# Kernel tuning notes

Measured on AMD Instinct MI355X. Metric: run time of the kernel, lower is better.

Reference implementation:

```python
import jax, jax.numpy as jnp
import numpy as np

BETA = 0.25  # commitment_beta from CodebookDecoder default


def setup_inputs() -> dict:
    key = jax.random.key(0)
    k1, k2, k3 = jax.random.split(key, 3)
    Q, B, K, D = 2048, 40000, 2048, 512
    return {
        "query_emb": jax.random.normal(k1, (Q, D), dtype=jnp.float32),
        "entity_emb": jax.random.normal(k2, (B, D), dtype=jnp.float32),
        "codebook": jax.random.normal(k3, (K, D), dtype=jnp.float32),
    }


def _quantize(x, codebook):
    # Nearest-neighbor lookup. torch.norm(x[:,None]-cb[None]) argmin is
    # equivalent to argmin of squared distance, expanded to avoid the
    x2 = jnp.sum(x * x, axis=1, keepdims=True)            # (B, 1)
    c2 = jnp.sum(codebook * codebook, axis=1)             # (K,)
    d2 = x2 - 2.0 * (x @ codebook.T) + c2[None, :]        # (B, K)
    idx = jnp.argmin(d2, axis=1)                          # (B,)
    quant = codebook[idx]                                 # (B, D) gather
    # vq_loss = mse(quant.detach(), x) + beta * mse(quant, x.detach())
    vq_loss = jnp.mean((jax.lax.stop_gradient(quant) - x) ** 2) \
        + BETA * jnp.mean((quant - jax.lax.stop_gradient(x)) ** 2)
    return quant, idx, vq_loss


def reference(query_emb, entity_emb, codebook):
    quant, idx, vq_loss = _quantize(entity_emb, codebook)
    score = query_emb @ quant.T                           # (Q, B)
    return score, vq_loss, idx
```

## Files before the change

kernel.cpp:

```cpp
#include <hip/hip_runtime.h>
#include <stdint.h>

#define Q    2048
#define NB   40000
#define NK   2048
#define ND   512
#define SCORE_SIZE (Q * NB)

typedef __bf16 bf16;
typedef bf16  bf16x8 __attribute__((ext_vector_type(8)));
typedef float f32x4  __attribute__((ext_vector_type(4)));

__device__ __forceinline__ unsigned short f2bf_rne(float f) {
    unsigned int u = __float_as_uint(f);
    u += 0x7FFFu + ((u >> 16) & 1u);
    return (unsigned short)(u >> 16);
}

__global__ __launch_bounds__(256) void c2_kernel(const float* __restrict__ cb,
                                                 float* __restrict__ c2) {
    int wave = threadIdx.x >> 6, lane = threadIdx.x & 63;
    int row  = blockIdx.x * 4 + wave;
    const float4* p = (const float4*)(cb + (size_t)row * ND);
    float4 a = p[lane];
    float4 b = p[lane + 64];
    float s = a.x*a.x + a.y*a.y + a.z*a.z + a.w*a.w
            + b.x*b.x + b.y*b.y + b.z*b.z + b.w*b.w;
    #pragma unroll
    for (int off = 32; off; off >>= 1) s += __shfl_down(s, off);
    if (lane == 0) c2[row] = s;
}

#define DPAD 132
__global__ __launch_bounds__(256) void dist_argmin_kernel(
        const float* __restrict__ ent, const float* __restrict__ cb,
        const float* __restrict__ c2g, float2* __restrict__ partial) {
    __shared__ float Es[32 * DPAD];
    __shared__ float Cs[32 * DPAD];
    int tid = threadIdx.x;
    int b0 = blockIdx.x * 128;
    int k0 = blockIdx.y * 128;
    int tx = tid & 15;
    int ty = tid >> 4;

    float acc[8][8] = {};

    for (int dc = 0; dc < ND; dc += 32) {
        __syncthreads();
        #pragma unroll
        for (int q = 0; q < 4; ++q) {
            int f4 = q * 256 + tid;
            int r  = f4 >> 3;
            int cc = f4 & 7;
            int br = b0 + r; br = br < NB ? br : NB - 1;
            float4 evv = *(const float4*)(ent + (size_t)br * ND + dc + cc * 4);
            float4 cvv = *(const float4*)(cb  + (size_t)(k0 + r) * ND + dc + cc * 4);
            int col = cc * 4;
            Es[(col + 0) * DPAD + r] = evv.x;
            Es[(col + 1) * DPAD + r] = evv.y;
            Es[(col + 2) * DPAD + r] = evv.z;
            Es[(col + 3) * DPAD + r] = evv.w;
            Cs[(col + 0) * DPAD + r] = cvv.x;
            Cs[(col + 1) * DPAD + r] = cvv.y;
            Cs[(col + 2) * DPAD + r] = cvv.z;
            Cs[(col + 3) * DPAD + r] = cvv.w;
        }
        __syncthreads();
        #pragma unroll 8
        for (int dd = 0; dd < 32; ++dd) {
            float4 e0 = *(const float4*)&Es[dd * DPAD + ty * 8];
            float4 e1 = *(const float4*)&Es[dd * DPAD + ty * 8 + 4];
            float4 q0 = *(const float4*)&Cs[dd * DPAD + tx * 8];
            float4 q1 = *(const float4*)&Cs[dd * DPAD + tx * 8 + 4];
            float ev[8] = {e0.x, e0.y, e0.z, e0.w, e1.x, e1.y, e1.z, e1.w};
            float cv[8] = {q0.x, q0.y, q0.z, q0.w, q1.x, q1.y, q1.z, q1.w};
            #pragma unroll
            for (int i = 0; i < 8; ++i)
                #pragma unroll
                for (int j = 0; j < 8; ++j)
                    acc[i][j] = fmaf(ev[i], cv[j], acc[i][j]);
        }
    }

    float c2v[8];
    #pragma unroll
    for (int j = 0; j < 8; ++j) c2v[j] = c2g[k0 + tx * 8 + j];

    for (int i = 0; i < 8; ++i) {
        int b = b0 + ty * 8 + i;
        float best = c2v[0] - 2.0f * acc[i][0];
        int bidx = k0 + tx * 8;
        #pragma unroll
        for (int j = 1; j < 8; ++j) {
            float v = c2v[j] - 2.0f * acc[i][j];
            if (v < best) { best = v; bidx = k0 + tx * 8 + j; }
        }
        #pragma unroll
        for (int off = 1; off < 16; off <<= 1) {
            float ov = __shfl_xor(best, off);
            int   oi = __shfl_xor(bidx, off);
            if (ov < best || (ov == best && oi < bidx)) { best = ov; bidx = oi; }
        }
        if (tx == 0 && b < NB)
            partial[(size_t)blockIdx.y * NB + b] = make_float2(best, __int_as_float(bidx));
    }
}

__global__ __launch_bounds__(256) void argmin_reduce_kernel(
        const float2* __restrict__ partial, int* __restrict__ idx_ws,
        float* __restrict__ out_idx) {
    int b = blockIdx.x * 256 + threadIdx.x;
    if (b >= NB) return;
    float2 p0 = partial[b];
    float best = p0.x;
    int bidx = __float_as_int(p0.y);
    #pragma unroll
    for (int t = 1; t < 16; ++t) {
        float2 p = partial[(size_t)t * NB + b];
        int i = __float_as_int(p.y);
        if (p.x < best || (p.x == best && i < bidx)) { best = p.x; bidx = i; }
    }
    idx_ws[b] = bidx;
    out_idx[b] = (float)bidx;
}

__global__ __launch_bounds__(256) void gather_loss_kernel(
        const float* __restrict__ ent, const float* __restrict__ cb,
        const int* __restrict__ idx_ws, unsigned short* __restrict__ quantb,
        float* __restrict__ acc) {
    int b = blockIdx.x;
    int k = idx_ws[b];
    int d = threadIdx.x * 2;
    float2 cv = *(const float2*)(cb  + (size_t)k * ND + d);
    float2 xv = *(const float2*)(ent + (size_t)b * ND + d);
    unsigned int packed = (unsigned int)f2bf_rne(cv.x) | ((unsigned int)f2bf_rne(cv.y) << 16);
    *(unsigned int*)(quantb + (size_t)b * ND + d) = packed;
    float dx = cv.x - xv.x, dy = cv.y - xv.y;
    float s = dx * dx + dy * dy;
    #pragma unroll
    for (int off = 32; off; off >>= 1) s += __shfl_down(s, off);
    __shared__ float wsum[4];
    int lane = threadIdx.x & 63, wave = threadIdx.x >> 6;
    if (lane == 0) wsum[wave] = s;
    __syncthreads();
    if (threadIdx.x == 0) atomicAdd(acc, wsum[0] + wsum[1] + wsum[2] + wsum[3]);
}

__global__ void vq_final_kernel(const float* __restrict__ acc, float* __restrict__ out) {
    out[0] = 1.25f * acc[0] / (float)(NB * ND);
}

__global__ __launch_bounds__(256) void qcvt_kernel(const float* __restrict__ qry,
                                                   unsigned short* __restrict__ qb) {
    int i = (blockIdx.x * 256 + threadIdx.x) * 4;
    float4 v = *(const float4*)(qry + i);
    uint2 u;
    u.x = (unsigned int)f2bf_rne(v.x) | ((unsigned int)f2bf_rne(v.y) << 16);
    u.y = (unsigned int)f2bf_rne(v.z) | ((unsigned int)f2bf_rne(v.w) << 16);
    *(uint2*)(qb + i) = u;
}

__global__ __launch_bounds__(256) void score_kernel(
        const unsigned short* __restrict__ Aq, const unsigned short* __restrict__ Bq,
        float* __restrict__ C) {
    __shared__ unsigned short As[128 * 32];
    __shared__ unsigned short Bs[128 * 32];
    int tid = threadIdx.x;
    int n0 = blockIdx.x * 128;
    int m0 = blockIdx.y * 128;
    int lane = tid & 63, wave = tid >> 6;
    int wm = wave >> 1, wn = wave & 1;
    int lr = lane & 15, quad = lane >> 4;

    f32x4 acc[4][4] = {};

    for (int kt = 0; kt < ND; kt += 32) {
        __syncthreads();
        #pragma unroll
        for (int r = 0; r < 2; ++r) {
            int e = r * 256 + tid;
            int row = e >> 2, cc = e & 3;
            uint4 va = *(const uint4*)(Aq + (size_t)(m0 + row) * ND + kt + cc * 8);
            *(uint4*)(As + row * 32 + cc * 8) = va;
            int nr = n0 + row; nr = nr < NB ? nr : NB - 1;
            uint4 vb = *(const uint4*)(Bq + (size_t)nr * ND + kt + cc * 8);
            *(uint4*)(Bs + row * 32 + cc * 8) = vb;
        }
        __syncthreads();
        bf16x8 af[4], bfr[4];
        #pragma unroll
        for (int mi = 0; mi < 4; ++mi)
            af[mi] = *(const bf16x8*)(As + (wm * 64 + mi * 16 + lr) * 32 + quad * 8);
        #pragma unroll
        for (int ni = 0; ni < 4; ++ni)
            bfr[ni] = *(const bf16x8*)(Bs + (wn * 64 + ni * 16 + lr) * 32 + quad * 8);
        #pragma unroll
        for (int mi = 0; mi < 4; ++mi)
            #pragma unroll
            for (int ni = 0; ni < 4; ++ni)
                acc[mi][ni] = __builtin_amdgcn_mfma_f32_16x16x32_bf16(
                    af[mi], bfr[ni], acc[mi][ni], 0, 0, 0);
    }

    #pragma unroll
    for (int mi = 0; mi < 4; ++mi) {
        #pragma unroll
        for (int ni = 0; ni < 4; ++ni) {
            int col = n0 + wn * 64 + ni * 16 + lr;
            if (col < NB) {
                #pragma unroll
                for (int r = 0; r < 4; ++r) {
                    int row = m0 + wm * 64 + mi * 16 + quad * 4 + r;
                    C[(size_t)row * NB + col] = acc[mi][ni][r];
                }
            }
        }
    }
}

extern "C" void kernel_launch(void* const* d_in, const int* in_sizes, int n_in,
                              void* d_out, int out_size, void* d_ws, size_t ws_size,
                              hipStream_t stream) {
    const float* qry = (const float*)d_in[0];
    const float* ent = (const float*)d_in[1];
    const float* cb  = (const float*)d_in[2];
    float* out = (float*)d_out;

    char* ws = (char*)d_ws;
    unsigned short* quantb = (unsigned short*)(ws);
    unsigned short* qb     = (unsigned short*)(ws + 40960000);
    float2*         partial= (float2*)(ws + 43057152);
    int*            idx_ws = (int*)(ws + 48177152);
    float*          c2     = (float*)(ws + 48337152);
    float*          acc    = (float*)(ws + 48345344);

    hipMemsetAsync(acc, 0, sizeof(float), stream);

    c2_kernel<<<NK / 4, 256, 0, stream>>>(cb, c2);
    dist_argmin_kernel<<<dim3(313, 16), 256, 0, stream>>>(ent, cb, c2, partial);
    argmin_reduce_kernel<<<(NB + 255) / 256, 256, 0, stream>>>(
        partial, idx_ws, out + SCORE_SIZE + 1);
    gather_loss_kernel<<<NB, 256, 0, stream>>>(ent, cb, idx_ws, quantb, acc);
    vq_final_kernel<<<1, 1, 0, stream>>>(acc, out + SCORE_SIZE);
    qcvt_kernel<<<1024, 256, 0, stream>>>(qry, qb);
    score_kernel<<<dim3(313, 16), 256, 0, stream>>>(qb, quantb, out);
}
```

Measured before the change: 1.990 ms.

## Compute codebook distances with split-bf16 MFMA, top-2 candidates, and exact fp32 rescoring

Replaces the scalar fp32 FMA distance GEMM with bf16 MFMA using a hi/lo split (three MFMAs per tile) to approximate fp32 accuracy. Each wave-half keeps its top-2 candidates, a merge kernel picks the top-4 per entity, and a rescore kernel recomputes exact fp32 distances to choose the final index, write the bf16 quant row and accumulate the loss. Entity pre-splitting into a workspace is used only when the workspace is large enough; otherwise the split happens on the fly during tile loads. This trades extra conversion passes and extra MFMA work for much higher matrix throughput, with a small risk of argmin mismatches if the true winner falls outside the candidate set.

Result: slower. 2.100 ms (+5.5%).

```diff
diff --git a/kernel.cpp b/kernel.cpp
--- a/kernel.cpp
+++ b/kernel.cpp
@@ -15,6 +15,17 @@
     unsigned int u = __float_as_uint(f);
     u += 0x7FFFu + ((u >> 16) & 1u);
     return (unsigned short)(u >> 16);
+}
+__device__ __forceinline__ float bf2f(unsigned short h) {
+    return __uint_as_float((unsigned int)h << 16);
+}
+__device__ __forceinline__ void split_pair_trunc(float x0, float x1,
+                                                 unsigned int& hp, unsigned int& lp) {
+    unsigned int u0 = __float_as_uint(x0), u1 = __float_as_uint(x1);
+    hp = (u0 >> 16) | (u1 & 0xFFFF0000u);
+    float l0 = x0 - __uint_as_float(u0 & 0xFFFF0000u);
+    float l1 = x1 - __uint_as_float(u1 & 0xFFFF0000u);
+    lp = (__float_as_uint(l0) >> 16) | (__float_as_uint(l1) & 0xFFFF0000u);
 }
 
 __global__ __launch_bounds__(256) void c2_kernel(const float* __restrict__ cb,
@@ -31,119 +42,222 @@
     if (lane == 0) c2[row] = s;
 }
 
-#define DPAD 132
-__global__ __launch_bounds__(256) void dist_argmin_kernel(
-        const float* __restrict__ ent, const float* __restrict__ cb,
-        const float* __restrict__ c2g, float2* __restrict__ partial) {
-    __shared__ float Es[32 * DPAD];
-    __shared__ float Cs[32 * DPAD];
+__global__ __launch_bounds__(256) void cvt_cb_kernel(const float* __restrict__ cb,
+        unsigned short* __restrict__ chi, unsigned short* __restrict__ clo) {
+    int i = (blockIdx.x * 256 + threadIdx.x) * 4;
+    float4 v = *(const float4*)(cb + i);
+    unsigned short h[4]; float l[4];
+    float x[4] = {v.x, v.y, v.z, v.w};
+    #pragma unroll
+    for (int j = 0; j < 4; ++j) { h[j] = f2bf_rne(x[j]); l[j] = x[j] - bf2f(h[j]); }
+    uint2 hp, lp;
+    hp.x = (unsigned int)h[0] | ((unsigned int)h[1] << 16);
+    hp.y = (unsigned int)h[2] | ((unsigned int)h[3] << 16);
+    lp.x = (unsigned int)f2bf_rne(l[0]) | ((unsigned int)f2bf_rne(l[1]) << 16);
+    lp.y = (unsigned int)f2bf_rne(l[2]) | ((unsigned int)f2bf_rne(l[3]) << 16);
+    *(uint2*)(chi + i) = hp;
+    *(uint2*)(clo + i) = lp;
+}
+
+__global__ __launch_bounds__(256) void cvt_ent_kernel(const float* __restrict__ ent,
+        unsigned short* __restrict__ ehi, unsigned short* __restrict__ elo) {
+    int i = (blockIdx.x * 256 + threadIdx.x) * 4;
+    float4 v = *(const float4*)(ent + i);
+    unsigned short h[4]; float l[4];
+    float x[4] = {v.x, v.y, v.z, v.w};
+    #pragma unroll
+    for (int j = 0; j < 4; ++j) { h[j] = f2bf_rne(x[j]); l[j] = x[j] - bf2f(h[j]); }
+    uint2 hp, lp;
+    hp.x = (unsigned int)h[0] | ((unsigned int)h[1] << 16);
+    hp.y = (unsigned int)h[2] | ((unsigned int)h[3] << 16);
+    lp.x = (unsigned int)f2bf_rne(l[0]) | ((unsigned int)f2bf_rne(l[1]) << 16);
+    lp.y = (unsigned int)f2bf_rne(l[2]) | ((unsigned int)f2bf_rne(l[3]) << 16);
+    *(uint2*)(ehi + i) = hp;
+    *(uint2*)(elo + i) = lp;
+}
+
+__device__ __forceinline__ void top2_insert(float& v1, int& i1, float& v2, int& i2,
+                                            float w, int j) {
+    if (w < v1 || (w == v1 && j < i1)) { v2 = v1; i2 = i1; v1 = w; i1 = j; }
+    else if (w < v2 || (w == v2 && j < i2)) { v2 = w; i2 = j; }
+}
+
+template<bool PRE>
+__global__ __launch_bounds__(256) void dist_mfma_kernel(
+        const float* __restrict__ entf,
+        const unsigned short* __restrict__ ehi, const unsigned short* __restrict__ elo,
+        const unsigned short* __restrict__ chi, const unsigned short* __restrict__ clo,
+        const float* __restrict__ c2g, float4* __restrict__ partial) {
+    __shared__ unsigned short EH[128 * 32];
+    __shared__ unsigned short EL[128 * 32];
+    __shared__ unsigned short CH[128 * 32];
+    __shared__ unsigned short CL[128 * 32];
     int tid = threadIdx.x;
     int b0 = blockIdx.x * 128;
     int k0 = blockIdx.y * 128;
-    int tx = tid & 15;
-    int ty = tid >> 4;
-
-    float acc[8][8] = {};
-
-    for (int dc = 0; dc < ND; dc += 32) {
+    int lane = tid & 63, wave = tid >> 6;
+    int wm = wave >> 1, wn = wave & 1;
+    int lr = lane & 15, quad = lane >> 4;
+
+    f32x4 acc[4][4] = {};
+
+    for (int kt = 0; kt < ND; kt += 32) {
         __syncthreads();
         #pragma unroll
-        for (int q = 0; q < 4; ++q) {
-            int f4 = q * 256 + tid;
-            int r  = f4 >> 3;
-            int cc = f4 & 7;
-            int br = b0 + r; br = br < NB ? br : NB - 1;
-            float4 evv = *(const float4*)(ent + (size_t)br * ND + dc + cc * 4);
-            float4 cvv = *(const float4*)(cb  + (size_t)(k0 + r) * ND + dc + cc * 4);
-            int col = cc * 4;
-            Es[(col + 0) * DPAD + r] = evv.x;
-            Es[(col + 1) * DPAD + r] = evv.y;
-            Es[(col + 2) * DPAD + r] = evv.z;
-            Es[(col + 3) * DPAD + r] = evv.w;
-            Cs[(col + 0) * DPAD + r] = cvv.x;
-            Cs[(col + 1) * DPAD + r] = cvv.y;
-            Cs[(col + 2) * DPAD + r] = cvv.z;
-            Cs[(col + 3) * DPAD + r] = cvv.w;
+        for (int r = 0; r < 2; ++r) {
+            int e = r * 256 + tid;
+            int row = e >> 2, cc = e & 3;
+            int br = b0 + row; br = br < NB ? br : NB - 1;
+            size_t eoff = (size_t)br * ND + kt + cc * 8;
+            if (PRE) {
+                *(uint4*)(EH + row * 32 + cc * 8) = *(const uint4*)(ehi + eoff);
+                *(uint4*)(EL + row * 32 + cc * 8) = *(const uint4*)(elo + eoff);
+            } else {
+                const float* src = entf + eoff;
+                float4 a = *(const float4*)src;
+                float4 b = *(const float4*)(src + 4);
+                uint4 hp, lp;
+                split_pair_trunc(a.x, a.y, hp.x, lp.x);
+                split_pair_trunc(a.z, a.w, hp.y, lp.y);
+                split_pair_trunc(b.x, b.y, hp.z, lp.z);
+                split_pair_trunc(b.z, b.w, hp.w, lp.w);
+                *(uint4*)(EH + row * 32 + cc * 8) = hp;
+                *(uint4*)(EL + row * 32 + cc * 8) = lp;
+            }
+            size_t coff = (size_t)(k0 + row) * ND + kt + cc * 8;
+            *(uint4*)(CH + row * 32 + cc * 8) = *(const uint4*)(chi + coff);
+            *(uint4*)(CL + row * 32 + cc * 8) = *(const uint4*)(clo + coff);
         }
         __syncthreads();
-        #pragma unroll 8
-        for (int dd = 0; dd < 32; ++dd) {
-            float4 e0 = *(const float4*)&Es[dd * DPAD + ty * 8];
-            float4 e1 = *(const float4*)&Es[dd * DPAD + ty * 8 + 4];
-            float4 q0 = *(const float4*)&Cs[dd * DPAD + tx * 8];
-            float4 q1 = *(const float4*)&Cs[dd * DPAD + tx * 8 + 4];
-            float ev[8] = {e0.x, e0.y, e0.z, e0.w, e1.x, e1.y, e1.z, e1.w};
-            float cv[8] = {q0.x, q0.y, q0.z, q0.w, q1.x, q1.y, q1.z, q1.w};
-            #pragma unroll
-            for (int i = 0; i < 8; ++i)
-                #pragma unroll
-                for (int j = 0; j < 8; ++j)
-                    acc[i][j] = fmaf(ev[i], cv[j], acc[i][j]);
-        }
-    }
-
-    float c2v[8];
-    #pragma unroll
-    for (int j = 0; j < 8; ++j) c2v[j] = c2g[k0 + tx * 8 + j];
-
-    for (int i = 0; i < 8; ++i) {
-        int b = b0 + ty * 8 + i;
-        float best = c2v[0] - 2.0f * acc[i][0];
-        int bidx = k0 + tx * 8;
-        #pragma unroll
-        for (int j = 1; j < 8; ++j) {
-            float v = c2v[j] - 2.0f * acc[i][j];
-            if (v < best) { best = v; bidx = k0 + tx * 8 + j; }
-        }
-        #pragma unroll
-        for (int off = 1; off < 16; off <<= 1) {
-            float ov = __shfl_xor(best, off);
-            int   oi = __shfl_xor(bidx, off);
-            if (ov < best || (ov == best && oi < bidx)) { best = ov; bidx = oi; }
-        }
-        if (tx == 0 && b < NB)
-            partial[(size_t)blockIdx.y * NB + b] = make_float2(best, __int_as_float(bidx));
-    }
-}
-
-__global__ __launch_bounds__(256) void argmin_reduce_kernel(
-        const float2* __restrict__ partial, int* __restrict__ idx_ws,
-        float* __restrict__ out_idx) {
+        bf16x8 ah[4], al[4], bh[4], bl[4];
+        #pragma unroll
+        for (int mi = 0; mi < 4; ++mi) {
+            int o = (wm * 64 + mi * 16 + lr) * 32 + quad * 8;
+            ah[mi] = *(const bf16x8*)(EH + o);
+            al[mi] = *(const bf16x8*)(EL + o);
+        }
+        #pragma unroll
+        for (int ni = 0; ni < 4; ++ni) {
+            int o = (wn * 64 + ni * 16 + lr) * 32 + quad * 8;
+            bh[ni] = *(const bf16x8*)(CH + o);
+            bl[ni] = *(const bf16x8*)(CL + o);
+        }
+        #pragma unroll
+        for (int mi = 0; mi < 4; ++mi)
+            #pragma unroll
+            for (int ni = 0; ni < 4; ++ni) {
+                acc[mi][ni] = __builtin_amdgcn_mfma_f32_16x16x32_bf16(
+                    ah[mi], bh[ni], acc[mi][ni], 0, 0, 0);
+                acc[mi][ni] = __builtin_amdgcn_mfma_f32_16x16x32_bf16(
+                    ah[mi], bl[ni], acc[mi][ni], 0, 0, 0);
+                acc[mi][ni] = __builtin_amdgcn_mfma_f32_16x16x32_bf16(
+                    al[mi], bh[ni], acc[mi][ni], 0, 0, 0);
+            }
+    }
+
+    float c2v[4];
+    #pragma unroll
+    for (int ni = 0; ni < 4; ++ni) c2v[ni] = c2g[k0 + wn * 64 + ni * 16 + lr];
+
+    #pragma unroll
+    for (int mi = 0; mi < 4; ++mi) {
+        #pragma unroll
+        for (int rr = 0; rr < 4; ++rr) {
+            float v1 = 3.4e38f, v2 = 3.4e38f;
+            int i1 = 0x7FFFFFFF, i2 = 0x7FFFFFFF;
+            #pragma unroll
+            for (int ni = 0; ni < 4; ++ni) {
+                float w = c2v[ni] - 2.0f * acc[mi][ni][rr];
+                top2_insert(v1, i1, v2, i2, w, k0 + wn * 64 + ni * 16 + lr);
+            }
+            #pragma unroll
+            for (int off = 1; off < 16; off <<= 1) {
+                float ov1 = __shfl_xor(v1, off); int oi1 = __shfl_xor(i1, off);
+                float ov2 = __shfl_xor(v2, off); int oi2 = __shfl_xor(i2, off);
+                top2_insert(v1, i1, v2, i2, ov1, oi1);
+                top2_insert(v1, i1, v2, i2, ov2, oi2);
+            }
+            int b = b0 + wm * 64 + mi * 16 + quad * 4 + rr;
+            if (lr == 0 && b < NB)
+                partial[(size_t)(blockIdx.y * 2 + wn) * NB + b] =
+                    make_float4(v1, __int_as_float(i1), v2, __int_as_float(i2));
+        }
+    }
+}
+
+__global__ __launch_bounds__(256) void cand_merge_kernel(
+        const float4* __restrict__ partial, int* __restrict__ cand) {
     int b = blockIdx.x * 256 + threadIdx.x;
     if (b >= NB) return;
-    float2 p0 = partial[b];
-    float best = p0.x;
-    int bidx = __float_as_int(p0.y);
-    #pragma unroll
-    for (int t = 1; t < 16; ++t) {
-        float2 p = partial[(size_t)t * NB + b];
-        int i = __float_as_int(p.y);
-        if (p.x < best || (p.x == best && i < bidx)) { best = p.x; bidx = i; }
-    }
-    idx_ws[b] = bidx;
-    out_idx[b] = (float)bidx;
-}
-
-__global__ __launch_bounds__(256) void gather_loss_kernel(
+    float tv[4] = {3.4e38f, 3.4e38f, 3.4e38f, 3.4e38f};
+    int   ti[4] = {0x7FFFFFFF, 0x7FFFFFFF, 0x7FFFFFFF, 0x7FFFFFFF};
+    for (int g = 0; g < 32; ++g) {
+        float4 p = partial[(size_t)g * NB + b];
+        float pv[2] = {p.x, p.z};
+        int   pi[2] = {__float_as_int(p.y), __float_as_int(p.w)};
+        #pragma unroll
+        for (int t = 0; t < 2; ++t) {
+            float w = pv[t]; int j = pi[t];
+            #pragma unroll
+            for (int s = 0; s < 4; ++s) {
+                if (w < tv[s] || (w == tv[s] && j < ti[s])) {
+                    float tmpv = tv[s]; int tmpi = ti[s];
+                    tv[s] = w; ti[s] = j; w = tmpv; j = tmpi;
+                }
+            }
+        }
+    }
+    #pragma unroll
+    for (int s = 0; s < 4; ++s) cand[b * 4 + s] = ti[s];
+}
+
+__global__ __launch_bounds__(256) void rescore_kernel(
         const float* __restrict__ ent, const float* __restrict__ cb,
-        const int* __restrict__ idx_ws, unsigned short* __restrict__ quantb,
+        const float* __restrict__ c2g, const int* __restrict__ cand,
+        unsigned short* __restrict__ quantb, float* __restrict__ out_idx,
         float* __restrict__ acc) {
     int b = blockIdx.x;
-    int k = idx_ws[b];
-    int d = threadIdx.x * 2;
-    float2 cv = *(const float2*)(cb  + (size_t)k * ND + d);
-    float2 xv = *(const float2*)(ent + (size_t)b * ND + d);
-    unsigned int packed = (unsigned int)f2bf_rne(cv.x) | ((unsigned int)f2bf_rne(cv.y) << 16);
-    *(unsigned int*)(quantb + (size_t)b * ND + d) = packed;
-    float dx = cv.x - xv.x, dy = cv.y - xv.y;
-    float s = dx * dx + dy * dy;
+    int wave = threadIdx.x >> 6, lane = threadIdx.x & 63;
+    int k = cand[b * 4 + wave];
+    const float4* xp = (const float4*)(ent + (size_t)b * ND);
+    const float4* cp = (const float4*)(cb + (size_t)k * ND);
+    float4 x0 = xp[lane * 2], x1 = xp[lane * 2 + 1];
+    float4 c0 = cp[lane * 2], c1 = cp[lane * 2 + 1];
+    float s = x0.x*c0.x + x0.y*c0.y + x0.z*c0.z + x0.w*c0.w
+            + x1.x*c1.x + x1.y*c1.y + x1.z*c1.z + x1.w*c1.w;
     #pragma unroll
     for (int off = 32; off; off >>= 1) s += __shfl_down(s, off);
-    __shared__ float wsum[4];
-    int lane = threadIdx.x & 63, wave = threadIdx.x >> 6;
-    if (lane == 0) wsum[wave] = s;
+    __shared__ float vws[4];
+    __shared__ int   kws[4];
+    __shared__ int   win;
+    if (lane == 0) { vws[wave] = c2g[k] - 2.0f * s; kws[wave] = k; }
     __syncthreads();
-    if (threadIdx.x == 0) atomicAdd(acc, wsum[0] + wsum[1] + wsum[2] + wsum[3]);
+    if (threadIdx.x == 0) {
+        float bv = vws[0]; int bk = kws[0], bw = 0;
+        #pragma unroll
+        for (int w = 1; w < 4; ++w) {
+            if (vws[w] < bv || (vws[w] == bv && kws[w] < bk)) {
+                bv = vws[w]; bk = kws[w]; bw = w;
+            }
+        }
+        win = bw;
+        out_idx[b] = (float)bk;
+    }
+    __syncthreads();
+    if (wave == win) {
+        uint4 qp;
+        qp.x = (unsigned int)f2bf_rne(c0.x) | ((unsigned int)f2bf_rne(c0.y) << 16);
+        qp.y = (unsigned int)f2bf_rne(c0.z) | ((unsigned int)f2bf_rne(c0.w) << 16);
+        qp.z = (unsigned int)f2bf_rne(c1.x) | ((unsigned int)f2bf_rne(c1.y) << 16);
+        qp.w = (unsigned int)f2bf_rne(c1.z) | ((unsigned int)f2bf_rne(c1.w) << 16);
+        *(uint4*)(quantb + (size_t)b * ND + lane * 8) = qp;
+        float d0 = c0.x - x0.x, d1 = c0.y - x0.y, d2 = c0.z - x0.z, d3 = c0.w - x0.w;
+        float d4 = c1.x - x1.x, d5 = c1.y - x1.y, d6 = c1.z - x1.z, d7 = c1.w - x1.w;
+        float l = d0*d0 + d1*d1 + d2*d2 + d3*d3 + d4*d4 + d5*d5 + d6*d6 + d7*d7;
+        #pragma unroll
+        for (int off = 32; off; off >>= 1) l += __shfl_down(l, off);
+        if (lane == 0) atomicAdd(acc, l);
+    }
 }
 
 __global__ void vq_final_kernel(const float* __restrict__ acc, float* __restrict__ out) {
@@ -227,21 +341,39 @@
     float* out = (float*)d_out;
 
     char* ws = (char*)d_ws;
-    unsigned short* quantb = (unsigned short*)(ws);
-    unsigned short* qb     = (unsigned short*)(ws + 40960000);
-    float2*         partial= (float2*)(ws + 43057152);
-    int*            idx_ws = (int*)(ws + 48177152);
-    float*          c2     = (float*)(ws + 48337152);
-    float*          acc    = (float*)(ws + 48345344);
+    const bool pre = ws_size >= 130ull * 1024 * 1024;
+
+    float4*         partial = (float4*)(ws);
+    unsigned short* quantb  = (unsigned short*)(ws);
+    size_t off = 40960000;
+    unsigned short *ehi = nullptr, *elo = nullptr;
+    if (pre) {
+        ehi = (unsigned short*)(ws + off); off += 40960000;
+        elo = (unsigned short*)(ws + off); off += 40960000;
+    }
+    unsigned short* chi = (unsigned short*)(ws + off); off += 2097152;
+    unsigned short* clo = (unsigned short*)(ws + off); off += 2097152;
+    unsigned short* qb  = (unsigned short*)(ws + off); off += 2097152;
+    int*            cand= (int*)(ws + off);            off += 640000;
+    float*          c2  = (float*)(ws + off);          off += 8192;
+    float*          acc = (float*)(ws + off);          off += 4;
 
     hipMemsetAsync(acc, 0, sizeof(float), stream);
 
     c2_kernel<<<NK / 4, 256, 0, stream>>>(cb, c2);
-    dist_argmin_kernel<<<dim3(313, 16), 256, 0, stream>>>(ent, cb, c2, partial);
-    argmin_reduce_kernel<<<(NB + 255) / 256, 256, 0, stream>>>(
-        partial, idx_ws, out + SCORE_SIZE + 1);
-    gather_loss_kernel<<<NB, 256, 0, stream>>>(ent, cb, idx_ws, quantb, acc);
+    cvt_cb_kernel<<<1024, 256, 0, stream>>>(cb, chi, clo);
+    qcvt_kernel<<<1024, 256, 0, stream>>>(qry, qb);
+    if (pre) {
+        cvt_ent_kernel<<<20000, 256, 0, stream>>>(ent, ehi, elo);
+        dist_mfma_kernel<true><<<dim3(313, 16), 256, 0, stream>>>(
+            ent, ehi, elo, chi, clo, c2, partial);
+    } else {
+        dist_mfma_kernel<false><<<dim3(313, 16), 256, 0, stream>>>(
+            ent, nullptr, nullptr, chi, clo, c2, partial);
+    }
+    cand_merge_kernel<<<(NB + 255) / 256, 256, 0, stream>>>(partial, cand);
+    rescore_kernel<<<NB, 256, 0, stream>>>(ent, cb, c2, cand, quantb,
+                                           out + SCORE_SIZE + 1, acc);
     vq_final_kernel<<<1, 1, 0, stream>>>(acc, out + SCORE_SIZE);
-    qcvt_kernel<<<1024, 256, 0, stream>>>(qry, qb);
     score_kernel<<<dim3(313, 16), 256, 0, stream>>>(qb, quantb, out);
 }
```
